# Kernel optimization log

Hardware: AMD Instinct MI355X
Metric: run time of the kernel (lower is better)

Reference implementation:

```python
import jax, jax.numpy as jnp
import numpy as np

EPS = 1e-10

def conv1x1(x, W, b):
    # x:[B,C,H,W], W:[O,C], b:[O]
    return jnp.einsum('bchw,oc->bohw', x, W) + b[None, :, None, None]

def setup_inputs() -> dict:
    key = jax.random.key(0)
    ks = jax.random.split(key, 16)
    B, C, H, W = 8, 512, 32, 32
    R, heads = 4, 8
    s = 1.0 / np.sqrt(C)
    inp = {
        'x': jax.random.normal(ks[0], (B, C, H, W), jnp.float32),
        'u_q': jax.random.uniform(ks[1], (B, R, H, W), jnp.float32, minval=EPS, maxval=1.0),
        'u_k': jax.random.uniform(ks[2], (B, R, H, W), jnp.float32, minval=EPS, maxval=1.0),
        'wq_s': jax.random.normal(ks[3], (R, C), jnp.float32) * s,
        'bq_s': jnp.zeros((R,), jnp.float32),
        'wk_s': jax.random.normal(ks[4], (R, C), jnp.float32) * s,
        'bk_s': jnp.zeros((R,), jnp.float32),
        'Wq': jax.random.normal(ks[5], (C, C), jnp.float32) * s,
        'bq': jnp.zeros((C,), jnp.float32),
        'Wk': jax.random.normal(ks[6], (C, C), jnp.float32) * s,
        'bk': jnp.zeros((C,), jnp.float32),
        'Wv': jax.random.normal(ks[7], (C, C), jnp.float32) * s,
        'bv': jnp.zeros((C,), jnp.float32),
        'Wp': jax.random.normal(ks[8], (C, C), jnp.float32) * s,
        'bp': jnp.zeros((C,), jnp.float32),
    }
    return inp

def reference(x, u_q, u_k, wq_s, bq_s, wk_s, bk_s, Wq, bq, Wk, bk, Wv, bv, Wp, bp):
    B, C, H, W = x.shape
    heads = 8
    hd = C // heads
    scale = hd ** -0.5
    N = H * W

    # gumbel-softmax hard=True then take channel 0 == (argmax(logits+g, dim=1) == 0)
    def sel_mask(ws, bs, u):
        logits = conv1x1(x, ws, bs)                       # [B,R,H,W]
        g = -jnp.log(-jnp.log(u + EPS) + EPS)             # gumbel noise
        m = jnp.argmax(logits + g, axis=1) == 0           # [B,H,W] bool
        return m.reshape(B, N)

    mq = jax.lax.stop_gradient(sel_mask(wq_s, bq_s, u_q))  # selected query points
    mk = jax.lax.stop_gradient(sel_mask(wk_s, bk_s, u_k))  # selected key/value points

    q = conv1x1(x, Wq, bq).reshape(B, heads, hd, N)
    k = conv1x1(x, Wk, bk).reshape(B, heads, hd, N)
    v = conv1x1(x, Wv, bv).reshape(B, heads, hd, N)

    # attention restricted to selected key positions (softmax over masked set
    # == softmax over the gathered subset in the torch code)
    attn = jnp.einsum('bhdn,bhdm->bhnm', q * scale, k)     # [B,h,N,N]
    attn = jnp.where(mk[:, None, None, :], attn, -1e30)
    attn = jax.nn.softmax(attn, axis=-1)
    out = jnp.einsum('bhnm,bhdm->bhdn', attn, v)           # [B,h,hd,N]

    # scatter attention output back into v at the selected query positions
    v_new = jnp.where(mq[:, None, :], out.reshape(B, C, N), v.reshape(B, C, N))
    v_new = v_new.reshape(B, C, H, W)
    return conv1x1(v_new, Wp, bp)
```

## Files before the change

### kernel.cpp

```cpp
#include <hip/hip_runtime.h>
#include <hip/hip_bf16.h>

#define B_ 8
#define C_ 512
#define N_ 1024
#define HEADS_ 8
#define HD_ 64

using f32x4  = __attribute__((ext_vector_type(4))) float;
using bf16x8 = __attribute__((ext_vector_type(8))) __bf16;

__device__ __forceinline__ unsigned short f2bf(float f) {
  union { float f; unsigned u; } v; v.f = f;
  unsigned r = v.u + 0x7FFFu + ((v.u >> 16) & 1u);
  return (unsigned short)(r >> 16);
}

__device__ __forceinline__ void gload16(const void* g, void* l) {
  __builtin_amdgcn_global_load_lds(
      (const __attribute__((address_space(1))) unsigned int*)g,
      (__attribute__((address_space(3))) unsigned int*)l, 16, 0, 0);
}

__global__ __launch_bounds__(256) void k_convw(
    const float* __restrict__ wq, const float* __restrict__ wk,
    const float* __restrict__ wv, const float* __restrict__ wp,
    unsigned short* __restrict__ out) {
  int i = blockIdx.x * 256 + threadIdx.x;
  int mat = i >> 18, idx = i & 262143;
  const float* src = (mat == 0) ? wq : (mat == 1) ? wk : (mat == 2) ? wv : wp;
  out[i] = f2bf(src[idx]);
}

__global__ __launch_bounds__(256) void k_transpose_x(
    const float* __restrict__ x, unsigned short* __restrict__ xT) {
  __shared__ float tile[64][65];
  int n0 = blockIdx.x * 64, c0 = blockIdx.y * 64, b = blockIdx.z;
  int t = threadIdx.x, tr = t >> 2, tc = (t & 3) * 16;
  const float* src = x + ((size_t)b * C_ + c0) * N_ + n0;
#pragma unroll
  for (int i = 0; i < 4; i++) {
    float4 v4 = *(const float4*)(src + (size_t)tr * N_ + tc + i * 4);
    tile[tr][tc + i * 4 + 0] = v4.x; tile[tr][tc + i * 4 + 1] = v4.y;
    tile[tr][tc + i * 4 + 2] = v4.z; tile[tr][tc + i * 4 + 3] = v4.w;
  }
  __syncthreads();
  unsigned short* dst = xT + ((size_t)b * N_ + n0) * C_ + c0;
#pragma unroll
  for (int i = 0; i < 4; i++) {
    unsigned short o4[4];
#pragma unroll
    for (int j = 0; j < 4; j++) o4[j] = f2bf(tile[tc + i * 4 + j][tr]);
    unsigned lo = (unsigned)o4[0] | ((unsigned)o4[1] << 16);
    unsigned hi = (unsigned)o4[2] | ((unsigned)o4[3] << 16);
    uint2 u; u.x = lo; u.y = hi;
    *(uint2*)(dst + (size_t)tr * C_ + tc + i * 4) = u;
  }
}

__global__ __launch_bounds__(256) void k_mask(
    const float* __restrict__ x, const float* __restrict__ u_q, const float* __restrict__ u_k,
    const float* __restrict__ wqs, const float* __restrict__ bqs,
    const float* __restrict__ wks, const float* __restrict__ bks,
    unsigned int* __restrict__ sel) {
  __shared__ float wq_l[4][512];
  __shared__ float wk_l[4][512];
  __shared__ float part[8 * 32 * 9];
  int b = blockIdx.y;
  int n0 = blockIdx.x * 32;
  int t = threadIdx.x, nl = t & 31, ch = t >> 5;
  for (int i = t; i < 2048; i += 256) {
    wq_l[i >> 9][i & 511] = wqs[i];
    wk_l[i >> 9][i & 511] = wks[i];
  }
  __syncthreads();
  int cbase = ch * 64;
  const float* xp = x + ((size_t)b * C_ + cbase) * N_ + n0 + nl;
  float sq[4] = {0.f, 0.f, 0.f, 0.f};
  float sk[4] = {0.f, 0.f, 0.f, 0.f};
  for (int c = 0; c < 64; c++) {
    float xv = xp[(size_t)c * N_];
#pragma unroll
    for (int r = 0; r < 4; r++) {
      sq[r] = fmaf(wq_l[r][cbase + c], xv, sq[r]);
      sk[r] = fmaf(wk_l[r][cbase + c], xv, sk[r]);
    }
  }
  float* pp = part + (ch * 32 + nl) * 9;
#pragma unroll
  for (int r = 0; r < 4; r++) { pp[r] = sq[r]; pp[4 + r] = sk[r]; }
  __syncthreads();
  if (t < 32) {
    int n = n0 + t;
    float fq[4], fk[4];
#pragma unroll
    for (int r = 0; r < 4; r++) { fq[r] = bqs[r]; fk[r] = bks[r]; }
#pragma unroll
    for (int c2 = 0; c2 < 8; c2++) {
      const float* q2 = part + (c2 * 32 + t) * 9;
#pragma unroll
      for (int r = 0; r < 4; r++) { fq[r] += q2[r]; fk[r] += q2[4 + r]; }
    }
#pragma unroll
    for (int r = 0; r < 4; r++) {
      float uq = u_q[((size_t)b * 4 + r) * N_ + n];
      float uk = u_k[((size_t)b * 4 + r) * N_ + n];
      fq[r] += -logf(-logf(uq + 1e-10f) + 1e-10f);
      fk[r] += -logf(-logf(uk + 1e-10f) + 1e-10f);
    }
    bool selq = (fq[0] >= fq[1]) && (fq[0] >= fq[2]) && (fq[0] >= fq[3]);
    bool selk = (fk[0] >= fk[1]) && (fk[0] >= fk[2]) && (fk[0] >= fk[3]);
    sel[(size_t)b * N_ + n] = selq ? 1u : 0u;
    sel[(size_t)(B_ + b) * N_ + n] = selk ? 1u : 0u;
  }
}

__global__ __launch_bounds__(1024) void k_scan(
    const unsigned int* __restrict__ sel, unsigned int* __restrict__ idx,
    unsigned int* __restrict__ cnt) {
  int which = blockIdx.x, b = blockIdx.y;
  const unsigned int* s = sel + ((size_t)which * B_ + b) * N_;
  unsigned int* ip = idx + ((size_t)which * B_ + b) * N_;
  int t = threadIdx.x, lane = t & 63, w = t >> 6;
  __shared__ unsigned int wtot[16], woff[16], totsh;
  unsigned int f = s[t];
  unsigned long long bal = __ballot(f != 0);
  unsigned int wpre = __popcll(bal & ((1ull << lane) - 1ull));
  if (lane == 0) wtot[w] = (unsigned int)__popcll(bal);
  __syncthreads();
  if (t == 0) {
    unsigned int acc = 0;
#pragma unroll
    for (int i = 0; i < 16; i++) { woff[i] = acc; acc += wtot[i]; }
    totsh = acc;
    cnt[which * B_ + b] = acc;
  }
  __syncthreads();
  unsigned int tot = totsh;
  if (f) ip[woff[w] + wpre] = (unsigned int)t;
  if (t >= (int)tot) ip[t] = 0u;
}

template <int MODE>
__global__ __launch_bounds__(256) void k_gemm(
    const unsigned short* __restrict__ Wall, const unsigned short* __restrict__ Bt,
    const float* __restrict__ bias0, const float* __restrict__ bias1,
    const float* __restrict__ bias2,
    const unsigned int* __restrict__ idx, const unsigned int* __restrict__ cnt,
    void* __restrict__ outv) {
  __shared__ __align__(16) unsigned short a_lds[128 * 64];
  __shared__ __align__(16) unsigned short b_lds[128 * 64];
  int z = blockIdx.z;
  int mat = (MODE == 0) ? (z >> 3) : 0;
  int b   = (MODE == 0) ? (z & 7) : z;
  int n0 = blockIdx.x * 128;
  if (MODE == 0 && mat < 2 && n0 >= (int)cnt[mat * B_ + b]) return;
  const unsigned short* A = Wall + (size_t)mat * 262144;
  const float* bias = (mat == 0) ? bias0 : (mat == 1) ? bias1 : bias2;
  int m0 = blockIdx.y * 128;
  int t = threadIdx.x, wave = t >> 6, lane = t & 63;
  int wr = (wave >> 1) * 64, wc = (wave & 1) * 64;
  f32x4 acc[4][4] = {};
  int srow = t >> 3, spch = t & 7;
  int lch = spch ^ (srow & 7);
  const unsigned short* aptr[4];
  const unsigned short* bptr[4];
#pragma unroll
  for (int i = 0; i < 4; i++) {
    int row = srow + i * 32;
    aptr[i] = A + (size_t)(m0 + row) * C_ + lch * 8;
    int grow = n0 + row;
    int srcr = (MODE == 0 && mat < 2) ? (int)idx[((size_t)mat * B_ + b) * N_ + grow] : grow;
    bptr[i] = Bt + ((size_t)b * N_ + srcr) * C_ + lch * 8;
  }
  for (int kt = 0; kt < 8; kt++) {
    int k0 = kt * 64;
    __syncthreads();
#pragma unroll
    for (int i = 0; i < 4; i++) {
      gload16(aptr[i] + k0, (char*)a_lds + wave * 1024 + i * 4096);
      gload16(bptr[i] + k0, (char*)b_lds + wave * 1024 + i * 4096);
    }
    __syncthreads();
#pragma unroll
    for (int ks = 0; ks < 2; ks++) {
      bf16x8 af[4], bfr[4];
#pragma unroll
      for (int mi = 0; mi < 4; mi++) {
        int row = wr + mi * 16 + (lane & 15);
        int pch = (ks * 4 + (lane >> 4)) ^ (row & 7);
        af[mi] = *(const bf16x8*)(a_lds + row * 64 + pch * 8);
      }
#pragma unroll
      for (int ni = 0; ni < 4; ni++) {
        int row = wc + ni * 16 + (lane & 15);
        int pch = (ks * 4 + (lane >> 4)) ^ (row & 7);
        bfr[ni] = *(const bf16x8*)(b_lds + row * 64 + pch * 8);
      }
#pragma unroll
      for (int mi = 0; mi < 4; mi++)
#pragma unroll
        for (int ni = 0; ni < 4; ni++)
          acc[mi][ni] = __builtin_amdgcn_mfma_f32_16x16x32_bf16(af[mi], bfr[ni], acc[mi][ni], 0, 0, 0);
    }
  }
  if (MODE == 0) {
    unsigned short* outp = (unsigned short*)outv + (size_t)mat * B_ * N_ * C_ + (size_t)b * N_ * C_;
#pragma unroll
    for (int mi = 0; mi < 4; mi++) {
      int ob = m0 + wr + mi * 16 + ((lane >> 4) << 2);
      float bs[4];
#pragma unroll
      for (int r = 0; r < 4; r++) bs[r] = bias[ob + r];
#pragma unroll
      for (int ni = 0; ni < 4; ni++) {
        int n = n0 + wc + ni * 16 + (lane & 15);
        unsigned short o4[4];
#pragma unroll
        for (int r = 0; r < 4; r++) o4[r] = f2bf(acc[mi][ni][r] + bs[r]);
        unsigned lo = (unsigned)o4[0] | ((unsigned)o4[1] << 16);
        unsigned hi = (unsigned)o4[2] | ((unsigned)o4[3] << 16);
        uint2 u; u.x = lo; u.y = hi;
        *(uint2*)(outp + (size_t)n * C_ + ob) = u;
      }
    }
  } else {
    float* outp = (float*)outv + (size_t)b * C_ * N_;
#pragma unroll
    for (int mi = 0; mi < 4; mi++) {
      int ob = m0 + wr + mi * 16 + ((lane >> 4) << 2);
#pragma unroll
      for (int r = 0; r < 4; r++) {
        float bv = bias[ob + r];
#pragma unroll
        for (int ni = 0; ni < 4; ni++) {
          int n = n0 + wc + ni * 16 + (lane & 15);
          outp[(size_t)(ob + r) * N_ + n] = acc[mi][ni][r] + bv;
        }
      }
    }
  }
}

__global__ __launch_bounds__(256) void k_gather_vt(
    const unsigned short* __restrict__ vT, const unsigned int* __restrict__ idx,
    const unsigned int* __restrict__ cnt, unsigned short* __restrict__ vctr) {
  int b = blockIdx.z;
  unsigned int nk = cnt[B_ + b];
  int j0 = blockIdx.x * 64;
  if (j0 >= (int)nk) return;
  int c0 = blockIdx.y * 64;
  __shared__ unsigned short tile[64][72];
  int t = threadIdx.x, tr = t >> 2, tc = (t & 3) * 16;
  int jj = j0 + tr;
  bool valid = jj < (int)nk;
  unsigned int srow = valid ? idx[((size_t)B_ + b) * N_ + jj] : 0u;
  const unsigned short* src = vT + ((size_t)b * N_ + srow) * C_ + c0;
#pragma unroll
  for (int i = 0; i < 4; i++) {
    ushort4 v4 = {0, 0, 0, 0};
    if (valid) v4 = *(const ushort4*)(src + tc + i * 4);
    tile[tr][tc + i * 4 + 0] = v4.x; tile[tr][tc + i * 4 + 1] = v4.y;
    tile[tr][tc + i * 4 + 2] = v4.z; tile[tr][tc + i * 4 + 3] = v4.w;
  }
  __syncthreads();
  unsigned short* dst = vctr + ((size_t)b * C_ + c0) * N_ + j0;
#pragma unroll
  for (int i = 0; i < 4; i++) {
    unsigned short o4[4];
#pragma unroll
    for (int j = 0; j < 4; j++) o4[j] = tile[tc + i * 4 + j][tr];
    unsigned lo = (unsigned)o4[0] | ((unsigned)o4[1] << 16);
    unsigned hi = (unsigned)o4[2] | ((unsigned)o4[3] << 16);
    uint2 u; u.x = lo; u.y = hi;
    *(uint2*)(dst + (size_t)tr * N_ + tc + i * 4) = u;
  }
}

__global__ __launch_bounds__(256) void k_attn(
    const unsigned short* __restrict__ qc, const unsigned short* __restrict__ kc,
    const unsigned short* __restrict__ vctr, unsigned short* __restrict__ vnew,
    const unsigned int* __restrict__ idx, const unsigned int* __restrict__ cnt) {
  __shared__ __align__(16) unsigned short k_lds[64 * 64];
  __shared__ __align__(16) unsigned short v_lds[64 * 64];
  __shared__ __align__(16) unsigned short p_lds[4][16 * 72];
  int qt = blockIdx.x, h = blockIdx.y, b = blockIdx.z;
  unsigned int nq = cnt[b], nk = cnt[B_ + b];
  if (qt * 64 >= (int)nq) return;
  int t = threadIdx.x, wave = t >> 6, lane = t & 63;
  int q0 = qt * 64 + wave * 16;
  const unsigned short* qp =
      qc + ((size_t)b * N_ + q0 + (lane & 15)) * C_ + h * HD_ + ((lane >> 4) * 8);
  bf16x8 qf0 = *(const bf16x8*)qp;
  bf16x8 qf1 = *(const bf16x8*)(qp + 32);
  float mrow[4], lrow[4];
  f32x4 acc[4];
#pragma unroll
  for (int r = 0; r < 4; r++) { mrow[r] = -1e30f; lrow[r] = 0.f; }
#pragma unroll
  for (int d = 0; d < 4; d++) acc[d] = f32x4{0.f, 0.f, 0.f, 0.f};
  int srow = t >> 3, spch = t & 7;
  int nkt = ((int)nk + 63) >> 6;
  for (int kt = 0; kt < nkt; kt++) {
    int n0 = kt * 64;
    __syncthreads();
#pragma unroll
    for (int i = 0; i < 2; i++) {
      int row = srow + i * 32;
      int lch = spch ^ (row & 7);
      gload16(kc + ((size_t)b * N_ + n0 + row) * C_ + h * HD_ + lch * 8,
              (char*)k_lds + wave * 1024 + i * 4096);
      gload16(vctr + ((size_t)b * C_ + h * HD_ + row) * N_ + n0 + lch * 8,
              (char*)v_lds + wave * 1024 + i * 4096);
    }
    __syncthreads();
    f32x4 s[4];
#pragma unroll
    for (int nf = 0; nf < 4; nf++) {
      int row = nf * 16 + (lane & 15);
      f32x4 z = {0.f, 0.f, 0.f, 0.f};
      {
        int pch = ((lane >> 4)) ^ (row & 7);
        bf16x8 kf = *(const bf16x8*)(k_lds + row * 64 + pch * 8);
        z = __builtin_amdgcn_mfma_f32_16x16x32_bf16(qf0, kf, z, 0, 0, 0);
      }
      {
        int pch = (4 + (lane >> 4)) ^ (row & 7);
        bf16x8 kf = *(const bf16x8*)(k_lds + row * 64 + pch * 8);
        z = __builtin_amdgcn_mfma_f32_16x16x32_bf16(qf1, kf, z, 0, 0, 0);
      }
      float mv = ((n0 + row) < (int)nk) ? 0.f : -1e30f;
#pragma unroll
      for (int r = 0; r < 4; r++) s[nf][r] = z[r] * 0.125f + mv;
    }
    float alpha[4];
#pragma unroll
    for (int r = 0; r < 4; r++) {
      float mx = fmaxf(fmaxf(s[0][r], s[1][r]), fmaxf(s[2][r], s[3][r]));
      mx = fmaxf(mx, __shfl_xor(mx, 1));
      mx = fmaxf(mx, __shfl_xor(mx, 2));
      mx = fmaxf(mx, __shfl_xor(mx, 4));
      mx = fmaxf(mx, __shfl_xor(mx, 8));
      float mn = fmaxf(mrow[r], mx);
      alpha[r] = __expf(mrow[r] - mn);
      mrow[r] = mn;
      float rs = 0.f;
      int ql = ((lane >> 4) << 2) + r;
#pragma unroll
      for (int nf = 0; nf < 4; nf++) {
        float sv = s[nf][r];
        float p = (sv < -1e29f) ? 0.f : __expf(sv - mn);
        rs += p;
        p_lds[wave][ql * 72 + nf * 16 + (lane & 15)] = f2bf(p);
      }
      rs += __shfl_xor(rs, 1);
      rs += __shfl_xor(rs, 2);
      rs += __shfl_xor(rs, 4);
      rs += __shfl_xor(rs, 8);
      lrow[r] = lrow[r] * alpha[r] + rs;
    }
    bf16x8 pa0 = *(const bf16x8*)&p_lds[wave][(lane & 15) * 72 + ((lane >> 4) * 8)];
    bf16x8 pa1 = *(const bf16x8*)&p_lds[wave][(lane & 15) * 72 + 32 + ((lane >> 4) * 8)];
#pragma unroll
    for (int df = 0; df < 4; df++) {
#pragma unroll
      for (int r = 0; r < 4; r++) acc[df][r] *= alpha[r];
      int row = df * 16 + (lane & 15);
      int pch0 = ((lane >> 4)) ^ (row & 7);
      int pch1 = (4 + (lane >> 4)) ^ (row & 7);
      bf16x8 vf0 = *(const bf16x8*)(v_lds + row * 64 + pch0 * 8);
      bf16x8 vf1 = *(const bf16x8*)(v_lds + row * 64 + pch1 * 8);
      acc[df] = __builtin_amdgcn_mfma_f32_16x16x32_bf16(pa0, vf0, acc[df], 0, 0, 0);
      acc[df] = __builtin_amdgcn_mfma_f32_16x16x32_bf16(pa1, vf1, acc[df], 0, 0, 0);
    }
  }
#pragma unroll
  for (int r = 0; r < 4; r++) {
    int ii = q0 + ((lane >> 4) << 2) + r;
    if (ii < (int)nq) {
      unsigned int qrow = idx[(size_t)b * N_ + ii];
      float inv = 1.0f / lrow[r];
      unsigned short* dst = vnew + ((size_t)b * N_ + qrow) * C_ + h * HD_ + (lane & 15);
#pragma unroll
      for (int df = 0; df < 4; df++) dst[df * 16] = f2bf(acc[df][r] * inv);
    }
  }
}

extern "C" void kernel_launch(void* const* d_in, const int* in_sizes, int n_in,
                              void* d_out, int out_size, void* d_ws, size_t ws_size,
                              hipStream_t stream) {
  const float* x   = (const float*)d_in[0];
  const float* u_q = (const float*)d_in[1];
  const float* u_k = (const float*)d_in[2];
  const float* wqs = (const float*)d_in[3];
  const float* bqs = (const float*)d_in[4];
  const float* wks = (const float*)d_in[5];
  const float* bks = (const float*)d_in[6];
  const float* Wq  = (const float*)d_in[7];
  const float* bq  = (const float*)d_in[8];
  const float* Wk  = (const float*)d_in[9];
  const float* bk  = (const float*)d_in[10];
  const float* Wv  = (const float*)d_in[11];
  const float* bv  = (const float*)d_in[12];
  const float* Wp  = (const float*)d_in[13];
  const float* bp  = (const float*)d_in[14];

  char* ws = (char*)d_ws;
  unsigned short* xT   = (unsigned short*)(ws);
  unsigned short* wbf  = (unsigned short*)(ws + 8388608);
  unsigned short* qkv  = (unsigned short*)(ws + 10485760);
  unsigned short* qc   = qkv;
  unsigned short* kc   = qkv + (size_t)B_ * N_ * C_;
  unsigned short* vT   = kc + (size_t)B_ * N_ * C_;
  unsigned short* vctr = (unsigned short*)(ws + 35651584);
  unsigned int*   sel  = (unsigned int*)(ws + 44040192);
  unsigned int*   idx  = (unsigned int*)(ws + 44105728);
  unsigned int*   cnt  = (unsigned int*)(ws + 44171264);

  k_convw<<<dim3(4096), 256, 0, stream>>>(Wq, Wk, Wv, Wp, wbf);
  k_transpose_x<<<dim3(16, 8, 8), 256, 0, stream>>>(x, xT);
  k_mask<<<dim3(32, 8), 256, 0, stream>>>(x, u_q, u_k, wqs, bqs, wks, bks, sel);
  k_scan<<<dim3(2, 8), 1024, 0, stream>>>(sel, idx, cnt);
  k_gemm<0><<<dim3(8, 4, 24), 256, 0, stream>>>(wbf, xT, bq, bk, bv, idx, cnt, (void*)qkv);
  k_gather_vt<<<dim3(16, 8, 8), 256, 0, stream>>>(vT, idx, cnt, vctr);
  k_attn<<<dim3(16, 8, 8), 256, 0, stream>>>(qc, kc, vctr, vT, idx, cnt);
  k_gemm<1><<<dim3(8, 4, 8), 256, 0, stream>>>(wbf + 3 * 262144, vT, bp, bp, bp, idx, cnt, d_out);
}
```

Measured before the change: 177.7 us.

## Split attention keys across waves, double-buffer GEMM LDS, vectorize weight conversion

The attention kernel now gives each block 16 queries, with the four waves each handling a disjoint strided subset of keys. K and V are read straight from global memory instead of being staged in LDS, and the per-wave softmax partials are merged through shared memory. This quadruples the grid so more blocks are in flight. The GEMM gets double-buffered LDS, prefetching the next K tile while the current one is computed, and the weight conversion kernel now processes four elements per thread. The risks are uncoalesced direct global loads of K and V, and extra shared memory pressure from the double buffers that may reduce occupancy.

```diff
diff --git a/kernel.cpp b/kernel.cpp
--- a/kernel.cpp
+++ b/kernel.cpp
@@ -27,9 +27,13 @@
     const float* __restrict__ wv, const float* __restrict__ wp,
     unsigned short* __restrict__ out) {
   int i = blockIdx.x * 256 + threadIdx.x;
-  int mat = i >> 18, idx = i & 262143;
+  int mat = i >> 16, idx4 = i & 65535;
   const float* src = (mat == 0) ? wq : (mat == 1) ? wk : (mat == 2) ? wv : wp;
-  out[i] = f2bf(src[idx]);
+  float4 v = ((const float4*)src)[idx4];
+  unsigned lo = (unsigned)f2bf(v.x) | ((unsigned)f2bf(v.y) << 16);
+  unsigned hi = (unsigned)f2bf(v.z) | ((unsigned)f2bf(v.w) << 16);
+  uint2 u; u.x = lo; u.y = hi;
+  ((uint2*)out)[i] = u;
 }
 
 __global__ __launch_bounds__(256) void k_transpose_x(
@@ -148,8 +152,8 @@
     const float* __restrict__ bias2,
     const unsigned int* __restrict__ idx, const unsigned int* __restrict__ cnt,
     void* __restrict__ outv) {
-  __shared__ __align__(16) unsigned short a_lds[128 * 64];
-  __shared__ __align__(16) unsigned short b_lds[128 * 64];
+  __shared__ __align__(16) unsigned short a_lds[2][128 * 64];
+  __shared__ __align__(16) unsigned short b_lds[2][128 * 64];
   int z = blockIdx.z;
   int mat = (MODE == 0) ? (z >> 3) : 0;
   int b   = (MODE == 0) ? (z & 7) : z;
@@ -173,15 +177,23 @@
     int srcr = (MODE == 0 && mat < 2) ? (int)idx[((size_t)mat * B_ + b) * N_ + grow] : grow;
     bptr[i] = Bt + ((size_t)b * N_ + srcr) * C_ + lch * 8;
   }
+#define STAGE_(buf, kt) do { int k0_ = (kt) * 64;                                   \
+    _Pragma("unroll") for (int i_ = 0; i_ < 4; i_++) {                              \
+      gload16(aptr[i_] + k0_, (char*)a_lds + (buf) * 16384 + wave * 1024 + i_ * 4096); \
+      gload16(bptr[i_] + k0_, (char*)b_lds + (buf) * 16384 + wave * 1024 + i_ * 4096); \
+    } } while (0)
+  STAGE_(0, 0);
   for (int kt = 0; kt < 8; kt++) {
-    int k0 = kt * 64;
-    __syncthreads();
-#pragma unroll
-    for (int i = 0; i < 4; i++) {
-      gload16(aptr[i] + k0, (char*)a_lds + wave * 1024 + i * 4096);
-      gload16(bptr[i] + k0, (char*)b_lds + wave * 1024 + i * 4096);
-    }
-    __syncthreads();
+    int cur = kt & 1;
+    if (kt < 7) {
+      STAGE_(cur ^ 1, kt + 1);
+      asm volatile("s_waitcnt vmcnt(8)" ::: "memory");
+    } else {
+      asm volatile("s_waitcnt vmcnt(0)" ::: "memory");
+    }
+    __builtin_amdgcn_s_barrier();
+    const unsigned short* al = a_lds[cur];
+    const unsigned short* bl = b_lds[cur];
 #pragma unroll
     for (int ks = 0; ks < 2; ks++) {
       bf16x8 af[4], bfr[4];
@@ -189,13 +201,13 @@
       for (int mi = 0; mi < 4; mi++) {
         int row = wr + mi * 16 + (lane & 15);
         int pch = (ks * 4 + (lane >> 4)) ^ (row & 7);
-        af[mi] = *(const bf16x8*)(a_lds + row * 64 + pch * 8);
+        af[mi] = *(const bf16x8*)(al + row * 64 + pch * 8);
       }
 #pragma unroll
       for (int ni = 0; ni < 4; ni++) {
         int row = wc + ni * 16 + (lane & 15);
         int pch = (ks * 4 + (lane >> 4)) ^ (row & 7);
-        bfr[ni] = *(const bf16x8*)(b_lds + row * 64 + pch * 8);
+        bfr[ni] = *(const bf16x8*)(bl + row * 64 + pch * 8);
       }
 #pragma unroll
       for (int mi = 0; mi < 4; mi++)
@@ -203,7 +215,9 @@
         for (int ni = 0; ni < 4; ni++)
           acc[mi][ni] = __builtin_amdgcn_mfma_f32_16x16x32_bf16(af[mi], bfr[ni], acc[mi][ni], 0, 0, 0);
     }
-  }
+    __builtin_amdgcn_s_barrier();
+  }
+#undef STAGE_
   if (MODE == 0) {
     unsigned short* outp = (unsigned short*)outv + (size_t)mat * B_ * N_ * C_ + (size_t)b * N_ * C_;
 #pragma unroll
@@ -281,14 +295,14 @@
     const unsigned short* __restrict__ qc, const unsigned short* __restrict__ kc,
     const unsigned short* __restrict__ vctr, unsigned short* __restrict__ vnew,
     const unsigned int* __restrict__ idx, const unsigned int* __restrict__ cnt) {
-  __shared__ __align__(16) unsigned short k_lds[64 * 64];
-  __shared__ __align__(16) unsigned short v_lds[64 * 64];
   __shared__ __align__(16) unsigned short p_lds[4][16 * 72];
+  __shared__ float macc[4][16][65];
+  __shared__ float mml[4][2][16];
   int qt = blockIdx.x, h = blockIdx.y, b = blockIdx.z;
-  unsigned int nq = cnt[b], nk = cnt[B_ + b];
-  if (qt * 64 >= (int)nq) return;
+  int nq = (int)cnt[b], nk = (int)cnt[B_ + b];
+  int q0 = qt * 16;
+  if (q0 >= nq) return;
   int t = threadIdx.x, wave = t >> 6, lane = t & 63;
-  int q0 = qt * 64 + wave * 16;
   const unsigned short* qp =
       qc + ((size_t)b * N_ + q0 + (lane & 15)) * C_ + h * HD_ + ((lane >> 4) * 8);
   bf16x8 qf0 = *(const bf16x8*)qp;
@@ -299,37 +313,18 @@
   for (int r = 0; r < 4; r++) { mrow[r] = -1e30f; lrow[r] = 0.f; }
 #pragma unroll
   for (int d = 0; d < 4; d++) acc[d] = f32x4{0.f, 0.f, 0.f, 0.f};
-  int srow = t >> 3, spch = t & 7;
-  int nkt = ((int)nk + 63) >> 6;
-  for (int kt = 0; kt < nkt; kt++) {
-    int n0 = kt * 64;
-    __syncthreads();
-#pragma unroll
-    for (int i = 0; i < 2; i++) {
-      int row = srow + i * 32;
-      int lch = spch ^ (row & 7);
-      gload16(kc + ((size_t)b * N_ + n0 + row) * C_ + h * HD_ + lch * 8,
-              (char*)k_lds + wave * 1024 + i * 4096);
-      gload16(vctr + ((size_t)b * C_ + h * HD_ + row) * N_ + n0 + lch * 8,
-              (char*)v_lds + wave * 1024 + i * 4096);
-    }
-    __syncthreads();
+  for (int j0 = wave * 64; j0 < nk; j0 += 256) {
     f32x4 s[4];
 #pragma unroll
     for (int nf = 0; nf < 4; nf++) {
-      int row = nf * 16 + (lane & 15);
+      const unsigned short* kp =
+          kc + ((size_t)b * N_ + j0 + nf * 16 + (lane & 15)) * C_ + h * HD_ + ((lane >> 4) * 8);
+      bf16x8 kf0 = *(const bf16x8*)kp;
+      bf16x8 kf1 = *(const bf16x8*)(kp + 32);
       f32x4 z = {0.f, 0.f, 0.f, 0.f};
-      {
-        int pch = ((lane >> 4)) ^ (row & 7);
-        bf16x8 kf = *(const bf16x8*)(k_lds + row * 64 + pch * 8);
-        z = __builtin_amdgcn_mfma_f32_16x16x32_bf16(qf0, kf, z, 0, 0, 0);
-      }
-      {
-        int pch = (4 + (lane >> 4)) ^ (row & 7);
-        bf16x8 kf = *(const bf16x8*)(k_lds + row * 64 + pch * 8);
-        z = __builtin_amdgcn_mfma_f32_16x16x32_bf16(qf1, kf, z, 0, 0, 0);
-      }
-      float mv = ((n0 + row) < (int)nk) ? 0.f : -1e30f;
+      z = __builtin_amdgcn_mfma_f32_16x16x32_bf16(qf0, kf0, z, 0, 0, 0);
+      z = __builtin_amdgcn_mfma_f32_16x16x32_bf16(qf1, kf1, z, 0, 0, 0);
+      float mv = ((j0 + nf * 16 + (lane & 15)) < nk) ? 0.f : -1e30f;
 #pragma unroll
       for (int r = 0; r < 4; r++) s[nf][r] = z[r] * 0.125f + mv;
     }
@@ -365,24 +360,48 @@
     for (int df = 0; df < 4; df++) {
 #pragma unroll
       for (int r = 0; r < 4; r++) acc[df][r] *= alpha[r];
-      int row = df * 16 + (lane & 15);
-      int pch0 = ((lane >> 4)) ^ (row & 7);
-      int pch1 = (4 + (lane >> 4)) ^ (row & 7);
-      bf16x8 vf0 = *(const bf16x8*)(v_lds + row * 64 + pch0 * 8);
-      bf16x8 vf1 = *(const bf16x8*)(v_lds + row * 64 + pch1 * 8);
+      const unsigned short* vp =
+          vctr + ((size_t)b * C_ + h * HD_ + df * 16 + (lane & 15)) * N_ + j0 + ((lane >> 4) * 8);
+      bf16x8 vf0 = *(const bf16x8*)vp;
+      bf16x8 vf1 = *(const bf16x8*)(vp + 32);
       acc[df] = __builtin_amdgcn_mfma_f32_16x16x32_bf16(pa0, vf0, acc[df], 0, 0, 0);
       acc[df] = __builtin_amdgcn_mfma_f32_16x16x32_bf16(pa1, vf1, acc[df], 0, 0, 0);
     }
   }
 #pragma unroll
-  for (int r = 0; r < 4; r++) {
-    int ii = q0 + ((lane >> 4) << 2) + r;
-    if (ii < (int)nq) {
-      unsigned int qrow = idx[(size_t)b * N_ + ii];
-      float inv = 1.0f / lrow[r];
-      unsigned short* dst = vnew + ((size_t)b * N_ + qrow) * C_ + h * HD_ + (lane & 15);
-#pragma unroll
-      for (int df = 0; df < 4; df++) dst[df * 16] = f2bf(acc[df][r] * inv);
+  for (int df = 0; df < 4; df++)
+#pragma unroll
+    for (int r = 0; r < 4; r++)
+      macc[wave][((lane >> 4) << 2) + r][df * 16 + (lane & 15)] = acc[df][r];
+  if ((lane & 15) == 0) {
+#pragma unroll
+    for (int r = 0; r < 4; r++) {
+      mml[wave][0][((lane >> 4) << 2) + r] = mrow[r];
+      mml[wave][1][((lane >> 4) << 2) + r] = lrow[r];
+    }
+  }
+  __syncthreads();
+  {
+    int q = t >> 4, d0 = (t & 15) * 4;
+    float mg = fmaxf(fmaxf(mml[0][0][q], mml[1][0][q]), fmaxf(mml[2][0][q], mml[3][0][q]));
+    float lg = 0.f, o0 = 0.f, o1 = 0.f, o2 = 0.f, o3 = 0.f;
+#pragma unroll
+    for (int w = 0; w < 4; w++) {
+      float sc = __expf(mml[w][0][q] - mg);
+      lg += mml[w][1][q] * sc;
+      o0 += macc[w][q][d0 + 0] * sc;
+      o1 += macc[w][q][d0 + 1] * sc;
+      o2 += macc[w][q][d0 + 2] * sc;
+      o3 += macc[w][q][d0 + 3] * sc;
+    }
+    if (q0 + q < nq) {
+      unsigned int qrow = idx[(size_t)b * N_ + q0 + q];
+      float inv = 1.0f / lg;
+      unsigned short o4[4] = {f2bf(o0 * inv), f2bf(o1 * inv), f2bf(o2 * inv), f2bf(o3 * inv)};
+      unsigned lo = (unsigned)o4[0] | ((unsigned)o4[1] << 16);
+      unsigned hi = (unsigned)o4[2] | ((unsigned)o4[3] << 16);
+      uint2 u; u.x = lo; u.y = hi;
+      *(uint2*)(vnew + ((size_t)b * N_ + qrow) * C_ + h * HD_ + d0) = u;
     }
   }
 }
@@ -418,12 +437,12 @@
   unsigned int*   idx  = (unsigned int*)(ws + 44105728);
   unsigned int*   cnt  = (unsigned int*)(ws + 44171264);
 
-  k_convw<<<dim3(4096), 256, 0, stream>>>(Wq, Wk, Wv, Wp, wbf);
+  k_convw<<<dim3(1024), 256, 0, stream>>>(Wq, Wk, Wv, Wp, wbf);
   k_transpose_x<<<dim3(16, 8, 8), 256, 0, stream>>>(x, xT);
   k_mask<<<dim3(32, 8), 256, 0, stream>>>(x, u_q, u_k, wqs, bqs, wks, bks, sel);
   k_scan<<<dim3(2, 8), 1024, 0, stream>>>(sel, idx, cnt);
   k_gemm<0><<<dim3(8, 4, 24), 256, 0, stream>>>(wbf, xT, bq, bk, bv, idx, cnt, (void*)qkv);
   k_gather_vt<<<dim3(16, 8, 8), 256, 0, stream>>>(vT, idx, cnt, vctr);
-  k_attn<<<dim3(16, 8, 8), 256, 0, stream>>>(qc, kc, vctr, vT, idx, cnt);
+  k_attn<<<dim3(64, 8, 8), 256, 0, stream>>>(qc, kc, vctr, vT, idx, cnt);
   k_gemm<1><<<dim3(8, 4, 8), 256, 0, stream>>>(wbf + 3 * 262144, vT, bp, bp, bp, idx, cnt, d_out);
 }
```

After: 167.7 us. 1.06x faster.
